# Kernel tuning notes

Measured on AMD Instinct MI355X. Metric: run time of the kernel, lower is better.

The kernel has to match this reference:

```python
import jax, jax.numpy as jnp
import numpy as np

N_STEPS = 256          # ray-marching samples per ray
DENSITY_SCALE = 10.0   # sigma scale (extinction coefficient multiplier)
EPS = 1e-8


def _trilerp(grid, x, y, z):
    """Trilinear interpolation. grid: [D,H,W]; x,y,z: voxel coords ([...])."""
    D, H, W = grid.shape
    x0 = jnp.clip(jnp.floor(x), 0, W - 2).astype(jnp.int32)
    y0 = jnp.clip(jnp.floor(y), 0, H - 2).astype(jnp.int32)
    z0 = jnp.clip(jnp.floor(z), 0, D - 2).astype(jnp.int32)
    fx = jnp.clip(x - x0, 0.0, 1.0)
    fy = jnp.clip(y - y0, 0.0, 1.0)
    fz = jnp.clip(z - z0, 0.0, 1.0)
    x1, y1, z1 = x0 + 1, y0 + 1, z0 + 1
    c000 = grid[z0, y0, x0]; c001 = grid[z0, y0, x1]
    c010 = grid[z0, y1, x0]; c011 = grid[z0, y1, x1]
    c100 = grid[z1, y0, x0]; c101 = grid[z1, y0, x1]
    c110 = grid[z1, y1, x0]; c111 = grid[z1, y1, x1]
    c00 = c000 * (1 - fx) + c001 * fx
    c01 = c010 * (1 - fx) + c011 * fx
    c10 = c100 * (1 - fx) + c101 * fx
    c11 = c110 * (1 - fx) + c111 * fx
    c0 = c00 * (1 - fy) + c01 * fy
    c1 = c10 * (1 - fy) + c11 * fy
    return c0 * (1 - fz) + c1 * fz


def _transmittance(rays, grid):
    """rays: [N,6] (origin, direction); grid: [D,H,W] clamped densities in [0,1].
    Marches through the [-1,1]^3 box and returns per-ray transmittance [N]."""
    D, H, W = grid.shape
    o = rays[:, 0:3]                                  # [N,3]
    d = rays[:, 3:6]
    d = d / (jnp.linalg.norm(d, axis=-1, keepdims=True) + EPS)
    # ray-box intersection with the unit box [-1,1]^3 (safe reciprocal)
    inv_d = 1.0 / jnp.where(jnp.abs(d) < EPS, jnp.sign(d) * EPS + EPS, d)
    t_a = (-1.0 - o) * inv_d
    t_b = (1.0 - o) * inv_d
    tmin = jnp.max(jnp.minimum(t_a, t_b), axis=-1)    # [N]
    tmax = jnp.min(jnp.maximum(t_a, t_b), axis=-1)
    tmin = jnp.maximum(tmin, 0.0)
    valid = tmax > tmin
    seg = jnp.where(valid, tmax - tmin, 0.0)          # traversed length
    # midpoint sample positions along each ray: [N, S, 3]
    frac = (jnp.arange(N_STEPS, dtype=grid.dtype) + 0.5) / N_STEPS
    ts = tmin[:, None] + seg[:, None] * frac[None, :]          # [N,S]
    pos = o[:, None, :] + ts[:, :, None] * d[:, None, :]        # [N,S,3]
    # map [-1,1] -> voxel coordinates
    gx = (pos[..., 0] + 1.0) * 0.5 * (W - 1)
    gy = (pos[..., 1] + 1.0) * 0.5 * (H - 1)
    gz = (pos[..., 2] + 1.0) * 0.5 * (D - 1)
    sigma = _trilerp(grid, gx, gy, gz)                 # [N,S]
    dt = seg / N_STEPS                                 # [N]
    tau = DENSITY_SCALE * jnp.sum(sigma, axis=-1) * dt
    return jnp.where(valid, jnp.exp(-tau), 1.0)


def setup_inputs() -> dict:
    key = jax.random.key(0)
    k_rays, k_grid = jax.random.split(key)
    rays = jax.random.normal(k_rays, (65536, 6), dtype=jnp.float32)
    grid = jax.random.uniform(k_grid, (256, 256, 256), dtype=jnp.float32)
    return {"rays": rays, "Grid": grid}


def reference(rays, Grid):
    # TrainableCloud.forward: renderer(rays, clamp(Grid, 0, 1))
    return _transmittance(rays, jnp.clip(Grid, 0.0, 1.0))
```

## Files before the change

kernel.cpp:

```cpp
#include <hip/hip_runtime.h>
#include <hip/hip_fp16.h>
#include <math.h>
#include <stdint.h>

#define N_STEPS 256
#define DENSITY_SCALE 10.0f
#define REF_EPS 1e-8f

typedef uint32_t u32_a2 __attribute__((aligned(2)));
typedef uint2 uint2_a4 __attribute__((aligned(4)));

__device__ __forceinline__ float clip01(float v) {
    return fminf(fmaxf(v, 0.0f), 1.0f);
}

__device__ __forceinline__ float safe_inv(float d) {
    float denom = d;
    if (fabsf(d) < REF_EPS) {
        float s = (d > 0.0f) ? 1.0f : ((d < 0.0f) ? -1.0f : 0.0f);
        denom = s * REF_EPS + REF_EPS;
    }
    return 1.0f / denom;
}

__device__ __forceinline__ uint32_t q255(float v) {
    return (uint32_t)__float2int_rn(clip01(v) * 255.0f);
}

__global__ __launch_bounds__(256) void repack_quad_kernel(
    const float* __restrict__ g, uint32_t* __restrict__ quad, int* __restrict__ counter)
{
    if (blockIdx.x == 0 && threadIdx.x == 0) *counter = 0;
    int t = blockIdx.x * blockDim.x + threadIdx.x;
    int x4 = (t & 63) << 2;
    int zy = t >> 6;
    int z = zy >> 8;
    int y = zy & 255;
    int yp = (y == 255) ? y : y + 1;
    int zp = (z == 255) ? z : z + 1;
    float4 a = *(const float4*)(g + ((z  << 16) + (y  << 8) + x4));
    float4 b = *(const float4*)(g + ((z  << 16) + (yp << 8) + x4));
    float4 c = *(const float4*)(g + ((zp << 16) + (y  << 8) + x4));
    float4 d = *(const float4*)(g + ((zp << 16) + (yp << 8) + x4));
    uint4 o;
    o.x = q255(a.x) | (q255(b.x) << 8) | (q255(c.x) << 16) | (q255(d.x) << 24);
    o.y = q255(a.y) | (q255(b.y) << 8) | (q255(c.y) << 16) | (q255(d.y) << 24);
    o.z = q255(a.z) | (q255(b.z) << 8) | (q255(c.z) << 16) | (q255(d.z) << 24);
    o.w = q255(a.w) | (q255(b.w) << 8) | (q255(c.w) << 16) | (q255(d.w) << 24);
    *(uint4*)(quad + ((zy << 8) + x4)) = o;
}

__global__ __launch_bounds__(256) void setup_kernel(
    const float* __restrict__ rays, float* __restrict__ out,
    float* __restrict__ compactF, int* __restrict__ compactI,
    int* __restrict__ counter, int n_rays)
{
    int ray = blockIdx.x * blockDim.x + threadIdx.x;
    bool valid = false;
    float ox = 0, oy = 0, oz = 0, dx = 0, dy = 0, dz = 0, tmin = 0, seg = 0;

    if (ray < n_rays) {
        const float* r = rays + ray * 6;
        ox = r[0]; oy = r[1]; oz = r[2];
        dx = r[3]; dy = r[4]; dz = r[5];
        float nrm = sqrtf(dx*dx + dy*dy + dz*dz) + REF_EPS;
        float inv_n = 1.0f / nrm;
        dx *= inv_n; dy *= inv_n; dz *= inv_n;
        float ixv = safe_inv(dx), iyv = safe_inv(dy), izv = safe_inv(dz);
        float tax = (-1.0f - ox) * ixv, tbx = (1.0f - ox) * ixv;
        float tay = (-1.0f - oy) * iyv, tby = (1.0f - oy) * iyv;
        float taz = (-1.0f - oz) * izv, tbz = (1.0f - oz) * izv;
        tmin = fmaxf(fmaxf(fminf(tax, tbx), fminf(tay, tby)), fminf(taz, tbz));
        float tmax = fminf(fminf(fmaxf(tax, tbx), fmaxf(tay, tby)), fmaxf(taz, tbz));
        tmin = fmaxf(tmin, 0.0f);
        valid = tmax > tmin;
        seg = valid ? (tmax - tmin) : 0.0f;
    }

    unsigned long long mask = __ballot(valid);
    int lane = threadIdx.x & 63;
    int nbefore = __popcll(mask & ((1ull << lane) - 1ull));
    int total = __popcll(mask);
    int base = 0;
    if (lane == 0) base = atomicAdd(counter, total);
    base = __shfl(base, 0);

    if (valid) {
        int idx = base + nbefore;
        float4* dst = (float4*)(compactF + (size_t)idx * 8);
        dst[0] = make_float4(ox, oy, oz, dx);
        dst[1] = make_float4(dy, dz, tmin, seg);
        compactI[idx] = ray;
    } else if (ray < n_rays) {
        out[ray] = 1.0f;
    }
}

__global__ __launch_bounds__(256) void march_kernel(
    const float* __restrict__ compactF, const int* __restrict__ compactI,
    const int* __restrict__ counter, const uint32_t* __restrict__ quad,
    float* __restrict__ out)
{
    int gid = blockIdx.x * blockDim.x + threadIdx.x;
    int sub = gid & 7;
    int nvalid = *counter;
    int stride = (gridDim.x * blockDim.x) >> 3;

    for (int ray = gid >> 3; ray < nvalid; ray += stride) {
        const float4* c = (const float4*)(compactF + (size_t)ray * 8);
        float4 c0 = c[0], c1 = c[1];
        float ox = c0.x, oy = c0.y, oz = c0.z;
        float dx = c0.w, dy = c1.x, dz = c1.y;
        float tmin = c1.z, seg = c1.w;

        float sum = 0.0f;
        #pragma unroll 4
        for (int i = sub; i < N_STEPS; i += 8) {
            float frac = ((float)i + 0.5f) * (1.0f / (float)N_STEPS);
            float t = fmaf(seg, frac, tmin);
            float px = fmaf(t, dx, ox);
            float py = fmaf(t, dy, oy);
            float pz = fmaf(t, dz, oz);
            float gx = (px + 1.0f) * (0.5f * 255.0f);
            float gy = (py + 1.0f) * (0.5f * 255.0f);
            float gz = (pz + 1.0f) * (0.5f * 255.0f);

            float fx0 = floorf(gx), fy0 = floorf(gy), fz0 = floorf(gz);
            int x0 = (int)fminf(fmaxf(fx0, 0.0f), 254.0f);
            int y0 = (int)fminf(fmaxf(fy0, 0.0f), 254.0f);
            int z0 = (int)fminf(fmaxf(fz0, 0.0f), 254.0f);
            float fx = fminf(fmaxf(gx - (float)x0, 0.0f), 1.0f);
            float fy = fminf(fmaxf(gy - (float)y0, 0.0f), 1.0f);
            float fz = fminf(fmaxf(gz - (float)z0, 0.0f), 1.0f);

            int vidx = (z0 << 16) + (y0 << 8) + x0;
            uint2 v = *(const uint2_a4*)(quad + vidx);
            float c000 = (float)( v.x        & 0xffu);
            float c010 = (float)((v.x >>  8) & 0xffu);
            float c100 = (float)((v.x >> 16) & 0xffu);
            float c110 = (float)( v.x >> 24        );
            float c001 = (float)( v.y        & 0xffu);
            float c011 = (float)((v.y >>  8) & 0xffu);
            float c101 = (float)((v.y >> 16) & 0xffu);
            float c111 = (float)( v.y >> 24        );

            float omfx = 1.0f - fx;
            float c00 = c000 * omfx + c001 * fx;
            float c01 = c010 * omfx + c011 * fx;
            float c10 = c100 * omfx + c101 * fx;
            float c11 = c110 * omfx + c111 * fx;
            float omfy = 1.0f - fy;
            float cc0 = c00 * omfy + c01 * fy;
            float cc1 = c10 * omfy + c11 * fy;
            sum += cc0 * (1.0f - fz) + cc1 * fz;
        }

        sum += __shfl_xor(sum, 1);
        sum += __shfl_xor(sum, 2);
        sum += __shfl_xor(sum, 4);

        if (sub == 0) {
            float dt = seg * (1.0f / (float)N_STEPS);
            float tau = (DENSITY_SCALE / 255.0f) * sum * dt;
            out[compactI[ray]] = expf(-tau);
        }
    }
}

__global__ __launch_bounds__(256) void repack_kernel(
    const float* __restrict__ g, __half* __restrict__ gh, int n)
{
    int i = (blockIdx.x * blockDim.x + threadIdx.x) * 4;
    if (i >= n) return;
    float4 v = *(const float4*)(g + i);
    __half2* dst = (__half2*)(gh + i);
    dst[0] = __floats2half2_rn(clip01(v.x), clip01(v.y));
    dst[1] = __floats2half2_rn(clip01(v.z), clip01(v.w));
}

__global__ __launch_bounds__(256) void transmittance_h_kernel(
    const float* __restrict__ rays, const __half* __restrict__ gh,
    float* __restrict__ out, int n_rays)
{
    int gid = blockIdx.x * blockDim.x + threadIdx.x;
    int ray = gid >> 3;
    int sub = gid & 7;
    if (ray >= n_rays) return;

    const float* r = rays + ray * 6;
    float ox = r[0], oy = r[1], oz = r[2];
    float dx = r[3], dy = r[4], dz = r[5];
    float nrm = sqrtf(dx*dx + dy*dy + dz*dz) + REF_EPS;
    float inv_n = 1.0f / nrm;
    dx *= inv_n; dy *= inv_n; dz *= inv_n;
    float ixv = safe_inv(dx), iyv = safe_inv(dy), izv = safe_inv(dz);
    float tax = (-1.0f - ox) * ixv, tbx = (1.0f - ox) * ixv;
    float tay = (-1.0f - oy) * iyv, tby = (1.0f - oy) * iyv;
    float taz = (-1.0f - oz) * izv, tbz = (1.0f - oz) * izv;
    float tmin = fmaxf(fmaxf(fminf(tax, tbx), fminf(tay, tby)), fminf(taz, tbz));
    float tmax = fminf(fminf(fmaxf(tax, tbx), fmaxf(tay, tby)), fmaxf(taz, tbz));
    tmin = fmaxf(tmin, 0.0f);
    bool valid = tmax > tmin;
    float seg = valid ? (tmax - tmin) : 0.0f;
    float sum = 0.0f;

    if (valid) {
        #pragma unroll 4
        for (int i = sub; i < N_STEPS; i += 8) {
            float frac = ((float)i + 0.5f) * (1.0f / (float)N_STEPS);
            float t = fmaf(seg, frac, tmin);
            float px = fmaf(t, dx, ox);
            float py = fmaf(t, dy, oy);
            float pz = fmaf(t, dz, oz);
            float gx = (px + 1.0f) * (0.5f * 255.0f);
            float gy = (py + 1.0f) * (0.5f * 255.0f);
            float gz = (pz + 1.0f) * (0.5f * 255.0f);
            float fx0 = floorf(gx), fy0 = floorf(gy), fz0 = floorf(gz);
            int x0 = (int)fminf(fmaxf(fx0, 0.0f), 254.0f);
            int y0 = (int)fminf(fmaxf(fy0, 0.0f), 254.0f);
            int z0 = (int)fminf(fmaxf(fz0, 0.0f), 254.0f);
            float fx = fminf(fmaxf(gx - (float)x0, 0.0f), 1.0f);
            float fy = fminf(fmaxf(gy - (float)y0, 0.0f), 1.0f);
            float fz = fminf(fmaxf(gz - (float)z0, 0.0f), 1.0f);
            const __half* p0 = gh + ((z0 << 16) + (y0 << 8) + x0);
            u32_a2 a00 = *(const u32_a2*)(const void*)(p0);
            u32_a2 a01 = *(const u32_a2*)(const void*)(p0 + 256);
            u32_a2 a10 = *(const u32_a2*)(const void*)(p0 + 65536);
            u32_a2 a11 = *(const u32_a2*)(const void*)(p0 + 65536 + 256);
            float2 f00 = __half22float2(*(__half2*)&a00);
            float2 f01 = __half22float2(*(__half2*)&a01);
            float2 f10 = __half22float2(*(__half2*)&a10);
            float2 f11 = __half22float2(*(__half2*)&a11);
            float omfx = 1.0f - fx;
            float c00 = f00.x * omfx + f00.y * fx;
            float c01 = f01.x * omfx + f01.y * fx;
            float c10 = f10.x * omfx + f10.y * fx;
            float c11 = f11.x * omfx + f11.y * fx;
            float omfy = 1.0f - fy;
            float cc0 = c00 * omfy + c01 * fy;
            float cc1 = c10 * omfy + c11 * fy;
            sum += cc0 * (1.0f - fz) + cc1 * fz;
        }
    }

    sum += __shfl_xor(sum, 1);
    sum += __shfl_xor(sum, 2);
    sum += __shfl_xor(sum, 4);

    if (sub == 0) {
        float result = 1.0f;
        if (valid) {
            float dt = seg * (1.0f / (float)N_STEPS);
            float tau = DENSITY_SCALE * sum * dt;
            result = expf(-tau);
        }
        out[ray] = result;
    }
}

__global__ __launch_bounds__(256) void transmittance_kernel(
    const float* __restrict__ rays, const float* __restrict__ grid,
    float* __restrict__ out, int n_rays)
{
    int gid = blockIdx.x * blockDim.x + threadIdx.x;
    int ray = gid >> 2;
    int sub = gid & 3;
    if (ray >= n_rays) return;
    const float* r = rays + ray * 6;
    float ox = r[0], oy = r[1], oz = r[2];
    float dx = r[3], dy = r[4], dz = r[5];
    float nrm = sqrtf(dx*dx + dy*dy + dz*dz) + REF_EPS;
    float inv_n = 1.0f / nrm;
    dx *= inv_n; dy *= inv_n; dz *= inv_n;
    float ixv = safe_inv(dx), iyv = safe_inv(dy), izv = safe_inv(dz);
    float tax = (-1.0f - ox) * ixv, tbx = (1.0f - ox) * ixv;
    float tay = (-1.0f - oy) * iyv, tby = (1.0f - oy) * iyv;
    float taz = (-1.0f - oz) * izv, tbz = (1.0f - oz) * izv;
    float tmin = fmaxf(fmaxf(fminf(tax, tbx), fminf(tay, tby)), fminf(taz, tbz));
    float tmax = fminf(fminf(fmaxf(tax, tbx), fmaxf(tay, tby)), fmaxf(taz, tbz));
    tmin = fmaxf(tmin, 0.0f);
    bool valid = tmax > tmin;
    float result = 1.0f;
    float seg = valid ? (tmax - tmin) : 0.0f;
    float sum = 0.0f;
    if (valid) {
        #pragma unroll 4
        for (int i = sub; i < N_STEPS; i += 4) {
            float frac = ((float)i + 0.5f) * (1.0f / (float)N_STEPS);
            float t = fmaf(seg, frac, tmin);
            float px = fmaf(t, dx, ox);
            float py = fmaf(t, dy, oy);
            float pz = fmaf(t, dz, oz);
            float gx = (px + 1.0f) * (0.5f * 255.0f);
            float gy = (py + 1.0f) * (0.5f * 255.0f);
            float gz = (pz + 1.0f) * (0.5f * 255.0f);
            float fx0 = floorf(gx), fy0 = floorf(gy), fz0 = floorf(gz);
            int x0 = (int)fminf(fmaxf(fx0, 0.0f), 254.0f);
            int y0 = (int)fminf(fmaxf(fy0, 0.0f), 254.0f);
            int z0 = (int)fminf(fmaxf(fz0, 0.0f), 254.0f);
            float fx = fminf(fmaxf(gx - (float)x0, 0.0f), 1.0f);
            float fy = fminf(fmaxf(gy - (float)y0, 0.0f), 1.0f);
            float fz = fminf(fmaxf(gz - (float)z0, 0.0f), 1.0f);
            const float* p0 = grid + ((z0 << 16) + (y0 << 8) + x0);
            const float* p1 = p0 + 65536;
            float c000 = p0[0],   c001 = p0[1];
            float c010 = p0[256], c011 = p0[257];
            float c100 = p1[0],   c101 = p1[1];
            float c110 = p1[256], c111 = p1[257];
            float omfx = 1.0f - fx;
            float c00 = c000 * omfx + c001 * fx;
            float c01 = c010 * omfx + c011 * fx;
            float c10 = c100 * omfx + c101 * fx;
            float c11 = c110 * omfx + c111 * fx;
            float omfy = 1.0f - fy;
            float cc0 = c00 * omfy + c01 * fy;
            float cc1 = c10 * omfy + c11 * fy;
            sum += cc0 * (1.0f - fz) + cc1 * fz;
        }
    }
    sum += __shfl_xor(sum, 1);
    sum += __shfl_xor(sum, 2);
    if (valid) {
        float dt = seg * (1.0f / (float)N_STEPS);
        float tau = DENSITY_SCALE * sum * dt;
        result = expf(-tau);
    }
    if (sub == 0) out[ray] = result;
}

extern "C" void kernel_launch(void* const* d_in, const int* in_sizes, int n_in,
                              void* d_out, int out_size, void* d_ws, size_t ws_size,
                              hipStream_t stream) {
    const float* rays = (const float*)d_in[0];
    const float* grid = (const float*)d_in[1];
    float* out = (float*)d_out;
    int n_rays = in_sizes[0] / 6;
    int n_grid = in_sizes[1];

    const size_t QUAD_BYTES = (size_t)n_grid * 4;
    const size_t CF_BYTES   = (size_t)n_rays * 8 * 4;
    const size_t CI_BYTES   = (size_t)n_rays * 4;
    const size_t need_full  = QUAD_BYTES + CF_BYTES + CI_BYTES + 256;
    const size_t need_half  = (size_t)n_grid * 2;

    if (ws_size >= need_full) {
        uint32_t* quad    = (uint32_t*)d_ws;
        float*    compactF = (float*)((char*)d_ws + QUAD_BYTES);
        int*      compactI = (int*)((char*)d_ws + QUAD_BYTES + CF_BYTES);
        int*      counter  = (int*)((char*)d_ws + QUAD_BYTES + CF_BYTES + CI_BYTES);

        int rp_threads = n_grid / 4;
        repack_quad_kernel<<<(rp_threads + 255) / 256, 256, 0, stream>>>(grid, quad, counter);
        setup_kernel<<<(n_rays + 255) / 256, 256, 0, stream>>>(
            rays, out, compactF, compactI, counter, n_rays);
        march_kernel<<<1024, 256, 0, stream>>>(compactF, compactI, counter, quad, out);
    } else if (ws_size >= need_half) {
        __half* gh = (__half*)d_ws;
        int rp_threads = n_grid / 4;
        repack_kernel<<<(rp_threads + 255) / 256, 256, 0, stream>>>(grid, gh, n_grid);
        int total_threads = n_rays * 8;
        transmittance_h_kernel<<<(total_threads + 255) / 256, 256, 0, stream>>>(
            rays, gh, out, n_rays);
    } else {
        int total_threads = n_rays * 4;
        transmittance_kernel<<<(total_threads + 255) / 256, 256, 0, stream>>>(
            rays, grid, out, n_rays);
    }
}
```

Measured before the change: 179.6 us.

## Bin ray segments into 64 spatial bricks and march per brick with atomic accumulation

Splits the 256^3 grid into 4x4x4 bricks. The setup kernel clips each valid ray against every brick and appends it to a per-brick list. A brick-major march kernel then samples only the steps that fall inside its brick and atomically adds partial sums per ray, and a finalize kernel applies the exponent. The goal is better cache locality in the gathers, since each block works within one 64^3 sub-volume. The cost is a 64-iteration binning loop in setup, a 16 MB tile-list workspace, extra kernels, many float atomics, and possible sample loss at brick boundaries if the floor-based ownership check and the index-range clipping disagree.

```diff
diff --git a/kernel.cpp b/kernel.cpp
--- a/kernel.cpp
+++ b/kernel.cpp
@@ -6,6 +6,7 @@
 #define N_STEPS 256
 #define DENSITY_SCALE 10.0f
 #define REF_EPS 1e-8f
+#define TILE_CAP 65536
 
 typedef uint32_t u32_a2 __attribute__((aligned(2)));
 typedef uint2 uint2_a4 __attribute__((aligned(4)));
@@ -27,10 +28,32 @@
     return (uint32_t)__float2int_rn(clip01(v) * 255.0f);
 }
 
+__device__ __forceinline__ float tile_lo(int k) {
+    return (k == 0) ? -1e30f : ((64.0f * k - 0.25f) * (1.0f / 127.5f) - 1.0f);
+}
+__device__ __forceinline__ float tile_hi(int k) {
+    return (k == 3) ?  1e30f : ((64.0f * k + 64.25f) * (1.0f / 127.5f) - 1.0f);
+}
+__device__ __forceinline__ void axis_clip(float o, float d, float lo, float hi,
+                                          float& ta, float& tb) {
+    if (fabsf(d) > 1e-6f) {
+        float inv = 1.0f / d;
+        float t0 = (lo - o) * inv, t1 = (hi - o) * inv;
+        ta = fmaxf(ta, fminf(t0, t1));
+        tb = fminf(tb, fmaxf(t0, t1));
+    } else if (o < lo || o > hi) {
+        ta = 1e30f; tb = -1e30f;
+    }
+}
+
 __global__ __launch_bounds__(256) void repack_quad_kernel(
-    const float* __restrict__ g, uint32_t* __restrict__ quad, int* __restrict__ counter)
-{
-    if (blockIdx.x == 0 && threadIdx.x == 0) *counter = 0;
+    const float* __restrict__ g, uint32_t* __restrict__ quad,
+    int* __restrict__ counter, int* __restrict__ tileCnt)
+{
+    if (blockIdx.x == 0) {
+        if (threadIdx.x == 0) *counter = 0;
+        if (threadIdx.x < 64) tileCnt[threadIdx.x] = 0;
+    }
     int t = blockIdx.x * blockDim.x + threadIdx.x;
     int x4 = (t & 63) << 2;
     int zy = t >> 6;
@@ -50,10 +73,11 @@
     *(uint4*)(quad + ((zy << 8) + x4)) = o;
 }
 
-__global__ __launch_bounds__(256) void setup_kernel(
+__global__ __launch_bounds__(256) void setup_tiles_kernel(
     const float* __restrict__ rays, float* __restrict__ out,
     float* __restrict__ compactF, int* __restrict__ compactI,
-    int* __restrict__ counter, int n_rays)
+    int* __restrict__ counter, int* __restrict__ tileCnt,
+    uint32_t* __restrict__ tileList, float* __restrict__ acc, int n_rays)
 {
     int ray = blockIdx.x * blockDim.x + threadIdx.x;
     bool valid = false;
@@ -82,9 +106,170 @@
     int nbefore = __popcll(mask & ((1ull << lane) - 1ull));
     int total = __popcll(mask);
     int base = 0;
-    if (lane == 0) base = atomicAdd(counter, total);
+    if (lane == 0 && total) base = atomicAdd(counter, total);
     base = __shfl(base, 0);
-
+    int cidx = base + nbefore;
+
+    if (valid) {
+        float4* dst = (float4*)(compactF + (size_t)cidx * 8);
+        dst[0] = make_float4(ox, oy, oz, dx);
+        dst[1] = make_float4(dy, dz, tmin, seg);
+        compactI[cidx] = ray;
+        acc[cidx] = 0.0f;
+    } else if (ray < n_rays) {
+        out[ray] = 1.0f;
+    }
+
+    for (int t = 0; t < 64; ++t) {
+        bool hit = false;
+        if (valid) {
+            int ttx = t & 3, tty = (t >> 2) & 3, ttz = t >> 4;
+            float ta = tmin, tb = tmin + seg;
+            axis_clip(ox, dx, tile_lo(ttx), tile_hi(ttx), ta, tb);
+            axis_clip(oy, dy, tile_lo(tty), tile_hi(tty), ta, tb);
+            axis_clip(oz, dz, tile_lo(ttz), tile_hi(ttz), ta, tb);
+            hit = (tb >= ta);
+        }
+        unsigned long long m = __ballot(hit);
+        if (m == 0ull) continue;
+        int tot = __popcll(m);
+        int rank = __popcll(m & ((1ull << lane) - 1ull));
+        int tbase = 0;
+        if (lane == 0) tbase = atomicAdd(&tileCnt[t], tot);
+        tbase = __shfl(tbase, 0);
+        if (hit) tileList[(size_t)t * TILE_CAP + tbase + rank] = (uint32_t)cidx;
+    }
+}
+
+__global__ __launch_bounds__(256) void march_tiles_kernel(
+    const float* __restrict__ compactF, const int* __restrict__ tileCnt,
+    const uint32_t* __restrict__ tileList, const uint32_t* __restrict__ quad,
+    float* __restrict__ acc)
+{
+    int tile  = blockIdx.x & 63;
+    int chunk = blockIdx.x >> 6;
+    int tx = tile & 3, ty = (tile >> 2) & 3, tz = tile >> 4;
+    int group = threadIdx.x >> 3;
+    int sub   = threadIdx.x & 7;
+    int cnt = tileCnt[tile];
+    if (cnt > TILE_CAP) cnt = TILE_CAP;
+
+    float wlx = tile_lo(tx), whx = tile_hi(tx);
+    float wly = tile_lo(ty), why = tile_hi(ty);
+    float wlz = tile_lo(tz), whz = tile_hi(tz);
+
+    for (int e = chunk * 32 + group; e < cnt; e += 4096) {
+        int ridx = tileList[(size_t)tile * TILE_CAP + e];
+        const float4* c = (const float4*)(compactF + (size_t)ridx * 8);
+        float4 c0 = c[0], c1 = c[1];
+        float ox = c0.x, oy = c0.y, oz = c0.z;
+        float dx = c0.w, dy = c1.x, dz = c1.y;
+        float tmin = c1.z, seg = c1.w;
+        float step = seg * (1.0f / (float)N_STEPS);
+
+        float ta = tmin, tb = tmin + seg;
+        axis_clip(ox, dx, wlx, whx, ta, tb);
+        axis_clip(oy, dy, wly, why, ta, tb);
+        axis_clip(oz, dz, wlz, whz, ta, tb);
+        if (tb < ta) continue;
+
+        int i_lo = (int)ceilf((ta - tmin) / step - 0.5f - 1e-3f);
+        int i_hi = (int)floorf((tb - tmin) / step - 0.5f + 1e-3f);
+        i_lo = max(i_lo, 0);
+        i_hi = min(i_hi, N_STEPS - 1);
+
+        float sum = 0.0f;
+        for (int i = i_lo + sub; i <= i_hi; i += 8) {
+            float frac = ((float)i + 0.5f) * (1.0f / (float)N_STEPS);
+            float t = fmaf(seg, frac, tmin);
+            float px = fmaf(t, dx, ox);
+            float py = fmaf(t, dy, oy);
+            float pz = fmaf(t, dz, oz);
+            float gx = (px + 1.0f) * (0.5f * 255.0f);
+            float gy = (py + 1.0f) * (0.5f * 255.0f);
+            float gz = (pz + 1.0f) * (0.5f * 255.0f);
+            int x0 = (int)fminf(fmaxf(floorf(gx), 0.0f), 254.0f);
+            int y0 = (int)fminf(fmaxf(floorf(gy), 0.0f), 254.0f);
+            int z0 = (int)fminf(fmaxf(floorf(gz), 0.0f), 254.0f);
+            if (((x0 >> 6) != tx) | ((y0 >> 6) != ty) | ((z0 >> 6) != tz)) continue;
+            float fx = fminf(fmaxf(gx - (float)x0, 0.0f), 1.0f);
+            float fy = fminf(fmaxf(gy - (float)y0, 0.0f), 1.0f);
+            float fz = fminf(fmaxf(gz - (float)z0, 0.0f), 1.0f);
+
+            int vidx = (z0 << 16) + (y0 << 8) + x0;
+            uint2 v = *(const uint2_a4*)(quad + vidx);
+            float c000 = (float)( v.x        & 0xffu);
+            float c010 = (float)((v.x >>  8) & 0xffu);
+            float c100 = (float)((v.x >> 16) & 0xffu);
+            float c110 = (float)( v.x >> 24        );
+            float c001 = (float)( v.y        & 0xffu);
+            float c011 = (float)((v.y >>  8) & 0xffu);
+            float c101 = (float)((v.y >> 16) & 0xffu);
+            float c111 = (float)( v.y >> 24        );
+
+            float omfx = 1.0f - fx;
+            float c00 = c000 * omfx + c001 * fx;
+            float c01 = c010 * omfx + c011 * fx;
+            float c10 = c100 * omfx + c101 * fx;
+            float c11 = c110 * omfx + c111 * fx;
+            float omfy = 1.0f - fy;
+            float cc0 = c00 * omfy + c01 * fy;
+            float cc1 = c10 * omfy + c11 * fy;
+            sum += cc0 * (1.0f - fz) + cc1 * fz;
+        }
+
+        sum += __shfl_xor(sum, 1);
+        sum += __shfl_xor(sum, 2);
+        sum += __shfl_xor(sum, 4);
+        if (sub == 0 && sum != 0.0f) atomicAdd(&acc[ridx], sum);
+    }
+}
+
+__global__ __launch_bounds__(256) void finalize_kernel(
+    const float* __restrict__ compactF, const int* __restrict__ compactI,
+    const int* __restrict__ counter, const float* __restrict__ acc,
+    float* __restrict__ out)
+{
+    int r = blockIdx.x * blockDim.x + threadIdx.x;
+    if (r >= *counter) return;
+    float seg = compactF[(size_t)r * 8 + 7];
+    float dt = seg * (1.0f / (float)N_STEPS);
+    float tau = (DENSITY_SCALE / 255.0f) * acc[r] * dt;
+    out[compactI[r]] = expf(-tau);
+}
+
+__global__ __launch_bounds__(256) void setup_kernel(
+    const float* __restrict__ rays, float* __restrict__ out,
+    float* __restrict__ compactF, int* __restrict__ compactI,
+    int* __restrict__ counter, int n_rays)
+{
+    int ray = blockIdx.x * blockDim.x + threadIdx.x;
+    bool valid = false;
+    float ox = 0, oy = 0, oz = 0, dx = 0, dy = 0, dz = 0, tmin = 0, seg = 0;
+    if (ray < n_rays) {
+        const float* r = rays + ray * 6;
+        ox = r[0]; oy = r[1]; oz = r[2];
+        dx = r[3]; dy = r[4]; dz = r[5];
+        float nrm = sqrtf(dx*dx + dy*dy + dz*dz) + REF_EPS;
+        float inv_n = 1.0f / nrm;
+        dx *= inv_n; dy *= inv_n; dz *= inv_n;
+        float ixv = safe_inv(dx), iyv = safe_inv(dy), izv = safe_inv(dz);
+        float tax = (-1.0f - ox) * ixv, tbx = (1.0f - ox) * ixv;
+        float tay = (-1.0f - oy) * iyv, tby = (1.0f - oy) * iyv;
+        float taz = (-1.0f - oz) * izv, tbz = (1.0f - oz) * izv;
+        tmin = fmaxf(fmaxf(fminf(tax, tbx), fminf(tay, tby)), fminf(taz, tbz));
+        float tmax = fminf(fminf(fmaxf(tax, tbx), fmaxf(tay, tby)), fmaxf(taz, tbz));
+        tmin = fmaxf(tmin, 0.0f);
+        valid = tmax > tmin;
+        seg = valid ? (tmax - tmin) : 0.0f;
+    }
+    unsigned long long mask = __ballot(valid);
+    int lane = threadIdx.x & 63;
+    int nbefore = __popcll(mask & ((1ull << lane) - 1ull));
+    int total = __popcll(mask);
+    int base = 0;
+    if (lane == 0 && total) base = atomicAdd(counter, total);
+    base = __shfl(base, 0);
     if (valid) {
         int idx = base + nbefore;
         float4* dst = (float4*)(compactF + (size_t)idx * 8);
@@ -105,14 +290,12 @@
     int sub = gid & 7;
     int nvalid = *counter;
     int stride = (gridDim.x * blockDim.x) >> 3;
-
     for (int ray = gid >> 3; ray < nvalid; ray += stride) {
         const float4* c = (const float4*)(compactF + (size_t)ray * 8);
         float4 c0 = c[0], c1 = c[1];
         float ox = c0.x, oy = c0.y, oz = c0.z;
         float dx = c0.w, dy = c1.x, dz = c1.y;
         float tmin = c1.z, seg = c1.w;
-
         float sum = 0.0f;
         #pragma unroll 4
         for (int i = sub; i < N_STEPS; i += 8) {
@@ -124,15 +307,12 @@
             float gx = (px + 1.0f) * (0.5f * 255.0f);
             float gy = (py + 1.0f) * (0.5f * 255.0f);
             float gz = (pz + 1.0f) * (0.5f * 255.0f);
-
-            float fx0 = floorf(gx), fy0 = floorf(gy), fz0 = floorf(gz);
-            int x0 = (int)fminf(fmaxf(fx0, 0.0f), 254.0f);
-            int y0 = (int)fminf(fmaxf(fy0, 0.0f), 254.0f);
-            int z0 = (int)fminf(fmaxf(fz0, 0.0f), 254.0f);
+            int x0 = (int)fminf(fmaxf(floorf(gx), 0.0f), 254.0f);
+            int y0 = (int)fminf(fmaxf(floorf(gy), 0.0f), 254.0f);
+            int z0 = (int)fminf(fmaxf(floorf(gz), 0.0f), 254.0f);
             float fx = fminf(fmaxf(gx - (float)x0, 0.0f), 1.0f);
             float fy = fminf(fmaxf(gy - (float)y0, 0.0f), 1.0f);
             float fz = fminf(fmaxf(gz - (float)z0, 0.0f), 1.0f);
-
             int vidx = (z0 << 16) + (y0 << 8) + x0;
             uint2 v = *(const uint2_a4*)(quad + vidx);
             float c000 = (float)( v.x        & 0xffu);
@@ -143,7 +323,6 @@
             float c011 = (float)((v.y >>  8) & 0xffu);
             float c101 = (float)((v.y >> 16) & 0xffu);
             float c111 = (float)( v.y >> 24        );
-
             float omfx = 1.0f - fx;
             float c00 = c000 * omfx + c001 * fx;
             float c01 = c010 * omfx + c011 * fx;
@@ -154,107 +333,14 @@
             float cc1 = c10 * omfy + c11 * fy;
             sum += cc0 * (1.0f - fz) + cc1 * fz;
         }
-
         sum += __shfl_xor(sum, 1);
         sum += __shfl_xor(sum, 2);
         sum += __shfl_xor(sum, 4);
-
         if (sub == 0) {
             float dt = seg * (1.0f / (float)N_STEPS);
             float tau = (DENSITY_SCALE / 255.0f) * sum * dt;
             out[compactI[ray]] = expf(-tau);
         }
-    }
-}
-
-__global__ __launch_bounds__(256) void repack_kernel(
-    const float* __restrict__ g, __half* __restrict__ gh, int n)
-{
-    int i = (blockIdx.x * blockDim.x + threadIdx.x) * 4;
-    if (i >= n) return;
-    float4 v = *(const float4*)(g + i);
-    __half2* dst = (__half2*)(gh + i);
-    dst[0] = __floats2half2_rn(clip01(v.x), clip01(v.y));
-    dst[1] = __floats2half2_rn(clip01(v.z), clip01(v.w));
-}
-
-__global__ __launch_bounds__(256) void transmittance_h_kernel(
-    const float* __restrict__ rays, const __half* __restrict__ gh,
-    float* __restrict__ out, int n_rays)
-{
-    int gid = blockIdx.x * blockDim.x + threadIdx.x;
-    int ray = gid >> 3;
-    int sub = gid & 7;
-    if (ray >= n_rays) return;
-
-    const float* r = rays + ray * 6;
-    float ox = r[0], oy = r[1], oz = r[2];
-    float dx = r[3], dy = r[4], dz = r[5];
-    float nrm = sqrtf(dx*dx + dy*dy + dz*dz) + REF_EPS;
-    float inv_n = 1.0f / nrm;
-    dx *= inv_n; dy *= inv_n; dz *= inv_n;
-    float ixv = safe_inv(dx), iyv = safe_inv(dy), izv = safe_inv(dz);
-    float tax = (-1.0f - ox) * ixv, tbx = (1.0f - ox) * ixv;
-    float tay = (-1.0f - oy) * iyv, tby = (1.0f - oy) * iyv;
-    float taz = (-1.0f - oz) * izv, tbz = (1.0f - oz) * izv;
-    float tmin = fmaxf(fmaxf(fminf(tax, tbx), fminf(tay, tby)), fminf(taz, tbz));
-    float tmax = fminf(fminf(fmaxf(tax, tbx), fmaxf(tay, tby)), fmaxf(taz, tbz));
-    tmin = fmaxf(tmin, 0.0f);
-    bool valid = tmax > tmin;
-    float seg = valid ? (tmax - tmin) : 0.0f;
-    float sum = 0.0f;
-
-    if (valid) {
-        #pragma unroll 4
-        for (int i = sub; i < N_STEPS; i += 8) {
-            float frac = ((float)i + 0.5f) * (1.0f / (float)N_STEPS);
-            float t = fmaf(seg, frac, tmin);
-            float px = fmaf(t, dx, ox);
-            float py = fmaf(t, dy, oy);
-            float pz = fmaf(t, dz, oz);
-            float gx = (px + 1.0f) * (0.5f * 255.0f);
-            float gy = (py + 1.0f) * (0.5f * 255.0f);
-            float gz = (pz + 1.0f) * (0.5f * 255.0f);
-            float fx0 = floorf(gx), fy0 = floorf(gy), fz0 = floorf(gz);
-            int x0 = (int)fminf(fmaxf(fx0, 0.0f), 254.0f);
-            int y0 = (int)fminf(fmaxf(fy0, 0.0f), 254.0f);
-            int z0 = (int)fminf(fmaxf(fz0, 0.0f), 254.0f);
-            float fx = fminf(fmaxf(gx - (float)x0, 0.0f), 1.0f);
-            float fy = fminf(fmaxf(gy - (float)y0, 0.0f), 1.0f);
-            float fz = fminf(fmaxf(gz - (float)z0, 0.0f), 1.0f);
-            const __half* p0 = gh + ((z0 << 16) + (y0 << 8) + x0);
-            u32_a2 a00 = *(const u32_a2*)(const void*)(p0);
-            u32_a2 a01 = *(const u32_a2*)(const void*)(p0 + 256);
-            u32_a2 a10 = *(const u32_a2*)(const void*)(p0 + 65536);
-            u32_a2 a11 = *(const u32_a2*)(const void*)(p0 + 65536 + 256);
-            float2 f00 = __half22float2(*(__half2*)&a00);
-            float2 f01 = __half22float2(*(__half2*)&a01);
-            float2 f10 = __half22float2(*(__half2*)&a10);
-            float2 f11 = __half22float2(*(__half2*)&a11);
-            float omfx = 1.0f - fx;
-            float c00 = f00.x * omfx + f00.y * fx;
-            float c01 = f01.x * omfx + f01.y * fx;
-            float c10 = f10.x * omfx + f10.y * fx;
-            float c11 = f11.x * omfx + f11.y * fx;
-            float omfy = 1.0f - fy;
-            float cc0 = c00 * omfy + c01 * fy;
-            float cc1 = c10 * omfy + c11 * fy;
-            sum += cc0 * (1.0f - fz) + cc1 * fz;
-        }
-    }
-
-    sum += __shfl_xor(sum, 1);
-    sum += __shfl_xor(sum, 2);
-    sum += __shfl_xor(sum, 4);
-
-    if (sub == 0) {
-        float result = 1.0f;
-        if (valid) {
-            float dt = seg * (1.0f / (float)N_STEPS);
-            float tau = DENSITY_SCALE * sum * dt;
-            result = expf(-tau);
-        }
-        out[ray] = result;
     }
 }
 
@@ -294,10 +380,9 @@
             float gx = (px + 1.0f) * (0.5f * 255.0f);
             float gy = (py + 1.0f) * (0.5f * 255.0f);
             float gz = (pz + 1.0f) * (0.5f * 255.0f);
-            float fx0 = floorf(gx), fy0 = floorf(gy), fz0 = floorf(gz);
-            int x0 = (int)fminf(fmaxf(fx0, 0.0f), 254.0f);
-            int y0 = (int)fminf(fmaxf(fy0, 0.0f), 254.0f);
-            int z0 = (int)fminf(fmaxf(fz0, 0.0f), 254.0f);
+            int x0 = (int)fminf(fmaxf(floorf(gx), 0.0f), 254.0f);
+            int y0 = (int)fminf(fmaxf(floorf(gy), 0.0f), 254.0f);
+            int z0 = (int)fminf(fmaxf(floorf(gz), 0.0f), 254.0f);
             float fx = fminf(fmaxf(gx - (float)x0, 0.0f), 1.0f);
             float fy = fminf(fmaxf(gy - (float)y0, 0.0f), 1.0f);
             float fz = fminf(fmaxf(gz - (float)z0, 0.0f), 1.0f);
@@ -340,27 +425,42 @@
     const size_t QUAD_BYTES = (size_t)n_grid * 4;
     const size_t CF_BYTES   = (size_t)n_rays * 8 * 4;
     const size_t CI_BYTES   = (size_t)n_rays * 4;
-    const size_t need_full  = QUAD_BYTES + CF_BYTES + CI_BYTES + 256;
-    const size_t need_half  = (size_t)n_grid * 2;
-
-    if (ws_size >= need_full) {
-        uint32_t* quad    = (uint32_t*)d_ws;
-        float*    compactF = (float*)((char*)d_ws + QUAD_BYTES);
-        int*      compactI = (int*)((char*)d_ws + QUAD_BYTES + CF_BYTES);
-        int*      counter  = (int*)((char*)d_ws + QUAD_BYTES + CF_BYTES + CI_BYTES);
+    const size_t TL_BYTES   = (size_t)64 * TILE_CAP * 4;
+    const size_t ACC_BYTES  = (size_t)n_rays * 4;
+    const size_t TC_BYTES   = 64 * 4 + 64;
+    const size_t need_tiled = QUAD_BYTES + CF_BYTES + CI_BYTES + TL_BYTES + ACC_BYTES + TC_BYTES;
+    const size_t need_mono  = QUAD_BYTES + CF_BYTES + CI_BYTES + 256;
+
+    char* p = (char*)d_ws;
+    if (ws_size >= need_tiled) {
+        uint32_t* quad     = (uint32_t*)p;                 p += QUAD_BYTES;
+        float*    compactF = (float*)p;                    p += CF_BYTES;
+        int*      compactI = (int*)p;                      p += CI_BYTES;
+        uint32_t* tileList = (uint32_t*)p;                 p += TL_BYTES;
+        float*    acc      = (float*)p;                    p += ACC_BYTES;
+        int*      tileCnt  = (int*)p;                      p += 64 * 4;
+        int*      counter  = (int*)p;
 
         int rp_threads = n_grid / 4;
-        repack_quad_kernel<<<(rp_threads + 255) / 256, 256, 0, stream>>>(grid, quad, counter);
+        repack_quad_kernel<<<(rp_threads + 255) / 256, 256, 0, stream>>>(
+            grid, quad, counter, tileCnt);
+        setup_tiles_kernel<<<(n_rays + 255) / 256, 256, 0, stream>>>(
+            rays, out, compactF, compactI, counter, tileCnt, tileList, acc, n_rays);
+        march_tiles_kernel<<<64 * 128, 256, 0, stream>>>(
+            compactF, tileCnt, tileList, quad, acc);
+        finalize_kernel<<<(n_rays + 255) / 256, 256, 0, stream>>>(
+            compactF, compactI, counter, acc, out);
+    } else if (ws_size >= need_mono) {
+        uint32_t* quad     = (uint32_t*)p;                 p += QUAD_BYTES;
+        float*    compactF = (float*)p;                    p += CF_BYTES;
+        int*      compactI = (int*)p;                      p += CI_BYTES;
+        int*      counter  = (int*)p;
+        int rp_threads = n_grid / 4;
+        repack_quad_kernel<<<(rp_threads + 255) / 256, 256, 0, stream>>>(
+            grid, quad, counter, counter + 16);
         setup_kernel<<<(n_rays + 255) / 256, 256, 0, stream>>>(
             rays, out, compactF, compactI, counter, n_rays);
         march_kernel<<<1024, 256, 0, stream>>>(compactF, compactI, counter, quad, out);
-    } else if (ws_size >= need_half) {
-        __half* gh = (__half*)d_ws;
-        int rp_threads = n_grid / 4;
-        repack_kernel<<<(rp_threads + 255) / 256, 256, 0, stream>>>(grid, gh, n_grid);
-        int total_threads = n_rays * 8;
-        transmittance_h_kernel<<<(total_threads + 255) / 256, 256, 0, stream>>>(
-            rays, gh, out, n_rays);
     } else {
         int total_threads = n_rays * 4;
         transmittance_kernel<<<(total_threads + 255) / 256, 256, 0, stream>>>(
```

New measurement: 642.5 us. +257.8%, slower.
